# Kernel optimization log

Hardware: AMD Instinct MI355X
Metric: run time of the kernel (lower is better)

Reference implementation:

```python
import jax, jax.numpy as jnp
import numpy as np

DIM = 1024

def setup_inputs() -> dict:
    key = jax.random.key(0)
    k1, k2, k3, k4, k5 = jax.random.split(key, 5)
    x = jax.random.normal(k1, (8, 2048, DIM), dtype=jnp.float32)
    # nn.Linear-style params: W is [out, in], b is [out]
    s = 1.0 / np.sqrt(DIM)
    W1 = jax.random.uniform(k2, (DIM, DIM), jnp.float32, -s, s)
    b1 = jax.random.uniform(k3, (DIM,), jnp.float32, -s, s)
    W2 = jax.random.uniform(k4, (DIM, DIM), jnp.float32, -s, s)
    b2 = jax.random.uniform(k5, (DIM,), jnp.float32, -s, s)
    return {"x": x, "W1": W1, "b1": b1, "W2": W2, "b2": b2}

def reference(x, W1, b1, W2, b2):
    # NOTE: original module reuses linear_1 for BOTH V and Q (linear_3 unused)
    V = x @ W1.T + b1                      # [B,S,D]
    K = x @ W2.T + b2                      # [B,S,D]
    Q = x @ W1.T + b1                      # [B,S,D]
    scale = 1.0 / jnp.sqrt(jnp.float32(x.shape[-1]))
    scores = jnp.einsum('bkd,bqd->bkq', K, Q) * scale  # K @ Q^T, [B,S,S]
    attn = jax.nn.softmax(scores, axis=-1)
    out = jnp.einsum('bkq,bqd->bkd', attn, V)
    return out
```

## Files before the change

kernel.cpp:

```cpp
#include <hip/hip_runtime.h>
#include <hip/hip_fp16.h>
#include <cstdint>
#include <cstddef>

#define DIMK 1024
#define NBATCH 8
#define SEQ 2048

typedef _Float16 half8 __attribute__((ext_vector_type(8)));
typedef _Float16 half4_t __attribute__((ext_vector_type(4)));
typedef float float4_t __attribute__((ext_vector_type(4)));

__device__ __forceinline__ void gload16(const _Float16* g, _Float16* l) {
  __builtin_amdgcn_global_load_lds((const __attribute__((address_space(1))) void*)g,
                                   (__attribute__((address_space(3))) void*)l, 16, 0, 0);
}

#define BAR() asm volatile("s_barrier" ::: "memory")
#define LGKM(n) asm volatile("s_waitcnt lgkmcnt(" #n ")" ::: "memory")
#define VMW(n) asm volatile("s_waitcnt vmcnt(" #n ")" ::: "memory")
#define PRIO1() __builtin_amdgcn_s_setprio(1)
#define PRIO0() __builtin_amdgcn_s_setprio(0)
#define SCHED0() __builtin_amdgcn_sched_barrier(0)

__device__ __forceinline__ void gemm256_core(
    const char* __restrict__ Ab, const char* __restrict__ Bb,
    const int ldA, const int ldB, const int NT, _Float16* lds,
    float4_t (&acc)[8][4])
{
  const int tid = threadIdx.x;
  const int lane = tid & 63, wave = tid >> 6;
  const int warp_m = wave >> 2, warp_n = wave & 3;
  const int srow = lane >> 3;
  const int scb = ((lane & 7) ^ srow) << 4;
  const int c0 = wave * 2;
  const int fr = lane & 15, fg = lane >> 4, rsw = lane & 7;

  const int xo0 = (fg ^ rsw) << 3;
  const int xo1 = ((4 + fg) ^ rsw) << 3;
  const int aro = (warp_m * 64 + fr) * 64;
  const int bro = 16384 + (warp_n * 32 + fr) * 64;

  _Float16* const sA = lds + c0 * 512;
  _Float16* const sB = lds + 16384 + c0 * 512;
  const char* const gA = Ab + (size_t)(c0 * 8 + srow) * ldA + scb;
  const char* const gB = Bb + (size_t)(c0 * 8 + srow) * ldB + scb;
  const size_t ldA8 = (size_t)ldA * 8,   ldB8 = (size_t)ldB * 8;
  const size_t ldA128 = (size_t)ldA * 128, ldB128 = (size_t)ldB * 128;

  half8 AfLo[4][2], AfHi[4][2], Bf0[2][2], Bf1[2][2];

#define STG_A(pbuf, ob_, bot) do { \
    _Float16* _lb = sA + (pbuf) + ((bot) ? 8192 : 0); \
    const char* _g = gA + ((bot) ? ldA128 : 0) + (size_t)(ob_); \
    gload16((const _Float16*)_g, _lb); \
    gload16((const _Float16*)(_g + ldA8), _lb + 512); } while (0)
#define STG_B(pbuf, ob_, bot) do { \
    _Float16* _lb = sB + (pbuf) + ((bot) ? 8192 : 0); \
    const char* _g = gB + ((bot) ? ldB128 : 0) + (size_t)(ob_); \
    gload16((const _Float16*)_g, _lb); \
    gload16((const _Float16*)(_g + ldB8), _lb + 512); } while (0)

#define RDA(DST, pbase, g) do { \
    _Pragma("unroll") for (int m = 0; m < 4; ++m) { \
      DST[m][0] = *(const half8*)(lds + (pbase) + aro + (g) * 8192 + m * 1024 + xo0); \
      DST[m][1] = *(const half8*)(lds + (pbase) + aro + (g) * 8192 + m * 1024 + xo1); \
    } } while (0)
#define RDB(DST, pbase, g) do { \
    _Pragma("unroll") for (int n = 0; n < 2; ++n) { \
      DST[n][0] = *(const half8*)(lds + (pbase) + bro + (g) * 8192 + n * 1024 + xo0); \
      DST[n][1] = *(const half8*)(lds + (pbase) + bro + (g) * 8192 + n * 1024 + xo1); \
    } } while (0)

#define QUAD(gm, gn, AF, BF) do { \
    _Pragma("unroll") for (int m = 0; m < 4; ++m) \
    _Pragma("unroll") for (int n = 0; n < 2; ++n) \
    _Pragma("unroll") for (int kk = 0; kk < 2; ++kk) \
      acc[(gm) * 4 + m][(gn) * 2 + n] = __builtin_amdgcn_mfma_f32_16x16x32_f16( \
          AF[m][kk], BF[n][kk], acc[(gm) * 4 + m][(gn) * 2 + n], 0, 0, 0); \
  } while (0)

  STG_A(0, 0, 0); STG_B(0, 0, 0); STG_B(0, 0, 1); STG_A(0, 0, 1);
  STG_A(32768, 128, 0); STG_B(32768, 128, 0); STG_B(32768, 128, 1);
  VMW(8);
  BAR();
  RDA(AfLo, 0, 0);
  RDB(Bf0, 0, 0);

  int t = 0;
  for (; t + 2 < NT; ++t) {
    const int pb = (t & 1) << 15, pbn = pb ^ 32768;
    const int o1 = (t + 1) << 7, o2 = (t + 2) << 7;
    VMW(6);
    RDB(Bf1, pb, 1);
    LGKM(4); SCHED0();
    PRIO1(); QUAD(0, 0, AfLo, Bf0); PRIO0();
    STG_A(pbn, o1, 1);
    BAR();
    RDA(AfHi, pb, 1);
    LGKM(8); SCHED0();
    PRIO1(); QUAD(0, 1, AfLo, Bf1); PRIO0();
    STG_A(pb, o2, 0);
    BAR();
    VMW(6);
    LGKM(0); SCHED0();
    PRIO1(); QUAD(1, 1, AfHi, Bf1); PRIO0();
    STG_B(pb, o2, 0);
    BAR();
    PRIO1(); QUAD(1, 0, AfHi, Bf0); PRIO0();
    RDA(AfLo, pbn, 0);
    RDB(Bf0, pbn, 0);
    VMW(6);
    STG_B(pb, o2, 1);
    BAR();
  }
  {
    const int pb = (t & 1) << 15, pbn = pb ^ 32768;
    const int oL = (NT - 1) << 7;
    VMW(6);
    RDB(Bf1, pb, 1);
    LGKM(4); SCHED0();
    PRIO1(); QUAD(0, 0, AfLo, Bf0); PRIO0();
    STG_A(pbn, oL, 1);
    BAR();
    RDA(AfHi, pb, 1);
    LGKM(8); SCHED0();
    PRIO1(); QUAD(0, 1, AfLo, Bf1); PRIO0();
    BAR();
    LGKM(0); SCHED0();
    PRIO1(); QUAD(1, 1, AfHi, Bf1); PRIO0();
    PRIO1(); QUAD(1, 0, AfHi, Bf0); PRIO0();
    VMW(0);
    BAR();
  }
  {
    const int pb = ((NT - 1) & 1) << 15;
    RDA(AfLo, pb, 0); RDB(Bf0, pb, 0); RDB(Bf1, pb, 1);
    QUAD(0, 0, AfLo, Bf0); QUAD(0, 1, AfLo, Bf1);
    RDA(AfHi, pb, 1);
    QUAD(1, 1, AfHi, Bf1); QUAD(1, 0, AfHi, Bf0);
  }
#undef STG_A
#undef STG_B
#undef RDA
#undef RDB
#undef QUAD
}

#define ROW_LOCAL(mi) (warp_m * 64 + ((mi) & 3) * 16 + (((mi) >> 2) ? 128 : 0))
#define COL_LOCAL(nj) (warp_n * 32 + (((nj) & 1) ? 16 : 0) + (((nj) >> 1) ? 128 : 0))

__global__ __launch_bounds__(256) void prep_kernel(const float* __restrict__ x,
                                                   const float* __restrict__ W1,
                                                   const float* __restrict__ W2,
                                                   _Float16* __restrict__ xh,
                                                   _Float16* __restrict__ Wcat) {
  int i = blockIdx.x * 256 + threadIdx.x;
  if (i < 4194304) {
    float4_t v = ((const float4_t*)x)[i];
    half4_t h; h[0]=(_Float16)v[0]; h[1]=(_Float16)v[1]; h[2]=(_Float16)v[2]; h[3]=(_Float16)v[3];
    ((half4_t*)xh)[i] = h;
  } else if (i < 4456448) {
    int j = i - 4194304;
    float4_t v = ((const float4_t*)W1)[j];
    half4_t h; h[0]=(_Float16)v[0]; h[1]=(_Float16)v[1]; h[2]=(_Float16)v[2]; h[3]=(_Float16)v[3];
    ((half4_t*)Wcat)[j] = h;
  } else if (i < 4718592) {
    int j = i - 4456448;
    float4_t v = ((const float4_t*)W2)[j];
    half4_t h; h[0]=(_Float16)v[0]; h[1]=(_Float16)v[1]; h[2]=(_Float16)v[2]; h[3]=(_Float16)v[3];
    ((half4_t*)(Wcat + 1048576))[j] = h;
  }
}

__global__ __launch_bounds__(512, 2) void gemm_vk_kernel(
    const _Float16* __restrict__ xh, const _Float16* __restrict__ Wcat,
    const float* __restrict__ b1, const float* __restrict__ b2,
    _Float16* __restrict__ Vbuf, _Float16* __restrict__ Kbuf,
    _Float16* __restrict__ Vt) {
  __shared__ _Float16 lds[65536];
  const int tid = threadIdx.x, lane = tid & 63, wave = tid >> 6;
  const int warp_m = wave >> 2, warp_n = wave & 3;
  const int fr = lane & 15, rb = (lane >> 4) * 4;
  const int flat = blockIdx.x;
  const int wg = (flat & 7) * 64 + (flat >> 3);
  const int bm = wg >> 3, bn = wg & 7;
  const bool isV = bn < 4;
  const float* bias = isV ? b1 : b2;
  const int ncol0 = (bn & 3) * 256;
  float bv[4];
#pragma unroll
  for (int nj = 0; nj < 4; ++nj) bv[nj] = bias[ncol0 + COL_LOCAL(nj) + fr];

  float4_t acc[8][4] = {};
  gemm256_core((const char*)(xh + (size_t)bm * 256 * DIMK),
               (const char*)(Wcat + (size_t)bn * 256 * DIMK),
               DIMK * 2, DIMK * 2, DIMK / 64, lds, acc);

  _Float16* dst = isV ? Vbuf : Kbuf;
#pragma unroll
  for (int mi = 0; mi < 8; ++mi) {
    const int row = bm * 256 + ROW_LOCAL(mi) + rb;
#pragma unroll
    for (int nj = 0; nj < 4; ++nj) {
      const int col = ncol0 + COL_LOCAL(nj) + fr;
#pragma unroll
      for (int r = 0; r < 4; ++r)
        dst[(size_t)(row + r) * DIMK + col] = (_Float16)(acc[mi][nj][r] + bv[nj]);
    }
  }
  if (isV) {
    __syncthreads();
#pragma unroll
    for (int mi = 0; mi < 8; ++mi) {
      const int q0 = ROW_LOCAL(mi) + rb;
#pragma unroll
      for (int nj = 0; nj < 4; ++nj) {
        const int d = COL_LOCAL(nj) + fr;
        const float bb = bv[nj];
#pragma unroll
        for (int r = 0; r < 4; ++r) {
          const int q = q0 + r;
          lds[d * 256 + ((((q >> 3) ^ d) & 31) << 3) + (q & 7)] = (_Float16)(acc[mi][nj][r] + bb);
        }
      }
    }
    __syncthreads();
    const int b = bm >> 3, qb = (bm & 7) * 256;
    const size_t vtb = ((size_t)b * DIMK + ncol0) * SEQ + qb;
#pragma unroll
    for (int i = 0; i < 16; ++i) {
      const int idx = tid + i * 512;
      const int d = idx >> 5, G = idx & 31;
      half8 v = *(const half8*)(lds + d * 256 + (((G ^ d) & 31) << 3));
      *(half8*)(Vt + vtb + (size_t)d * SEQ + G * 8) = v;
    }
  }
}

__global__ __launch_bounds__(512, 2) void gemm_scores_kernel(
    const _Float16* __restrict__ Kb, const _Float16* __restrict__ Vb,
    _Float16* __restrict__ P, float* __restrict__ rsum_part) {
  __shared__ _Float16 lds[65536];
  const int tid = threadIdx.x, lane = tid & 63, wave = tid >> 6;
  const int warp_m = wave >> 2, warp_n = wave & 3;
  const int fr = lane & 15, rb = (lane >> 4) * 4;
  const int flat = blockIdx.x;
  const int wg = (flat & 7) * 64 + (flat >> 3);
  const int b = wg >> 6, loc = wg & 63, bm = loc >> 3, bn = loc & 7;

  float4_t acc[8][4] = {};
  gemm256_core((const char*)(Kb + (size_t)(b * SEQ + bm * 256) * DIMK),
               (const char*)(Vb + (size_t)(b * SEQ + bn * 256) * DIMK),
               DIMK * 2, DIMK * 2, DIMK / 64, lds, acc);

  __syncthreads();
  float* part = (float*)lds;
  _Float16* Pb = P + (size_t)b * SEQ * SEQ;
#pragma unroll
  for (int mi = 0; mi < 8; ++mi) {
    const int rl = ROW_LOCAL(mi) + rb;
#pragma unroll
    for (int r = 0; r < 4; ++r) {
      float s = 0.f;
#pragma unroll
      for (int nj = 0; nj < 4; ++nj) {
        const int col = bn * 256 + COL_LOCAL(nj) + fr;
        const _Float16 ph = (_Float16)__expf(acc[mi][nj][r] * 0.03125f);
        Pb[(size_t)(bm * 256 + rl + r) * SEQ + col] = ph;
        s += (float)ph;
      }
      s += __shfl_xor(s, 1, 64);
      s += __shfl_xor(s, 2, 64);
      s += __shfl_xor(s, 4, 64);
      s += __shfl_xor(s, 8, 64);
      if (fr == 0) part[warp_n * 256 + rl + r] = s;
    }
  }
  __syncthreads();
  if (tid < 256) {
    const float s = part[tid] + part[256 + tid] + part[512 + tid] + part[768 + tid];
    rsum_part[((size_t)b * 8 + bn) * SEQ + bm * 256 + tid] = s;
  }
}

__global__ __launch_bounds__(512, 2) void gemm_out_kernel(
    const _Float16* __restrict__ P, const _Float16* __restrict__ Vt,
    const float* __restrict__ rsum_part, float* __restrict__ out) {
  __shared__ _Float16 lds[65536];
  const int tid = threadIdx.x, lane = tid & 63, wave = tid >> 6;
  const int warp_m = wave >> 2, warp_n = wave & 3;
  const int fr = lane & 15, rb = (lane >> 4) * 4;
  const int flat = blockIdx.x;
  const int wg = (flat & 7) * 32 + (flat >> 3);
  const int b = wg >> 5, loc = wg & 31, bm = loc >> 2, bn = loc & 3;

  float4_t acc[8][4] = {};
  gemm256_core((const char*)(P + (size_t)(b * SEQ + bm * 256) * SEQ),
               (const char*)(Vt + (size_t)(b * DIMK + bn * 256) * SEQ),
               SEQ * 2, SEQ * 2, SEQ / 64, lds, acc);

  __syncthreads();
  float* invf = (float*)lds;
  if (tid < 256) {
    const float* rp = rsum_part + (size_t)b * 8 * SEQ + bm * 256 + tid;
    float s = 0.f;
#pragma unroll
    for (int j = 0; j < 8; ++j) s += rp[j * SEQ];
    invf[tid] = __builtin_amdgcn_rcpf(s);
  }
  __syncthreads();

  float* ob = out + ((size_t)b * SEQ + bm * 256) * DIMK + bn * 256;
#pragma unroll
  for (int mi = 0; mi < 8; ++mi) {
#pragma unroll
    for (int r = 0; r < 4; ++r) {
      const int row = ROW_LOCAL(mi) + rb + r;
      const float inv = invf[row];
#pragma unroll
      for (int nj = 0; nj < 4; ++nj) {
        const int col = COL_LOCAL(nj) + fr;
        ob[(size_t)row * DIMK + col] = acc[mi][nj][r] * inv;
      }
    }
  }
}

extern "C" void kernel_launch(void* const* d_in, const int* in_sizes, int n_in,
                              void* d_out, int out_size, void* d_ws, size_t ws_size,
                              hipStream_t stream) {
  const float* x  = (const float*)d_in[0];
  const float* W1 = (const float*)d_in[1];
  const float* b1 = (const float*)d_in[2];
  const float* W2 = (const float*)d_in[3];
  const float* b2 = (const float*)d_in[4];
  float* out = (float*)d_out;

  char* ws = (char*)d_ws;
  _Float16* xh   = (_Float16*)(ws);
  _Float16* Pbuf = (_Float16*)(ws);
  _Float16* Vt   = (_Float16*)(ws + 67108864);
  _Float16* Vbuf = (_Float16*)(ws + 100663296);
  _Float16* Kbuf = (_Float16*)(ws + 134217728);
  _Float16* Wcat = (_Float16*)(ws + 167772160);
  float* rsum_part = (float*)(ws + 167772160);

  prep_kernel<<<18432, 256, 0, stream>>>(x, W1, W2, xh, Wcat);
  gemm_vk_kernel<<<512, 512, 0, stream>>>(xh, Wcat, b1, b2, Vbuf, Kbuf, Vt);
  gemm_scores_kernel<<<512, 512, 0, stream>>>(Kbuf, Vbuf, Pbuf, rsum_part);
  gemm_out_kernel<<<256, 512, 0, stream>>>(Pbuf, Vt, rsum_part, out);
}
```

Measured before the change: 327.1 us.

## Unroll GEMM main loop by two with ping-pong B fragments and earlier LDS prefetch

Restructures the double-buffered GEMM main loop into a two-tile unrolled steady state that alternates the roles of the two B fragment register sets. LDS reads for the next tile's A and B fragments are issued earlier, interleaved with MFMA quads instead of after them, and the vmcnt waits are retuned. The epilogue is rewritten to match the new fragment rotation. The aim is to hide LDS read latency behind MFMA work, at the cost of more complex wait-count bookkeeping that could race if a count is wrong.

```diff
diff --git a/kernel.cpp b/kernel.cpp
--- a/kernel.cpp
+++ b/kernel.cpp
@@ -80,18 +80,50 @@
           AF[m][kk], BF[n][kk], acc[(gm) * 4 + m][(gn) * 2 + n], 0, 0, 0); \
   } while (0)
 
+#define TILE_STEADY(t_, BLO, BHI) do { \
+    const int pb = ((t_) & 1) << 15, pbn = pb ^ 32768; \
+    const int o1 = ((t_) + 1) << 7, o2 = ((t_) + 2) << 7; \
+     \
+    RDB(BHI, pb, 1); \
+    LGKM(4); SCHED0(); \
+    PRIO1(); QUAD(0, 0, AfLo, BLO); PRIO0(); \
+    STG_A(pbn, o1, 1); \
+    BAR(); \
+     \
+    RDA(AfHi, pb, 1); \
+    LGKM(8); SCHED0(); \
+    PRIO1(); QUAD(0, 1, AfLo, BHI); PRIO0(); \
+    STG_A(pb, o2, 0); \
+    VMW(6); \
+    BAR(); \
+     \
+    RDA(AfLo, pbn, 0); \
+    LGKM(8); SCHED0(); \
+    PRIO1(); QUAD(1, 1, AfHi, BHI); PRIO0(); \
+    STG_B(pb, o2, 0); \
+    BAR(); \
+     \
+    RDB(BHI, pbn, 0); \
+    PRIO1(); QUAD(1, 0, AfHi, BLO); PRIO0(); \
+    VMW(4); \
+    STG_B(pb, o2, 1); \
+    BAR(); \
+  } while (0)
+
   STG_A(0, 0, 0); STG_B(0, 0, 0); STG_B(0, 0, 1); STG_A(0, 0, 1);
   STG_A(32768, 128, 0); STG_B(32768, 128, 0); STG_B(32768, 128, 1);
-  VMW(8);
+  VMW(6);
   BAR();
   RDA(AfLo, 0, 0);
   RDB(Bf0, 0, 0);
 
-  int t = 0;
-  for (; t + 2 < NT; ++t) {
-    const int pb = (t & 1) << 15, pbn = pb ^ 32768;
-    const int o1 = (t + 1) << 7, o2 = (t + 2) << 7;
-    VMW(6);
+  for (int t = 0; t + 4 <= NT; t += 2) {
+    TILE_STEADY(t, Bf0, Bf1);
+    TILE_STEADY(t + 1, Bf1, Bf0);
+  }
+  {
+    const int pb = ((NT - 2) & 1) << 15, pbn = pb ^ 32768;
+    const int o1 = (NT - 1) << 7;
     RDB(Bf1, pb, 1);
     LGKM(4); SCHED0();
     PRIO1(); QUAD(0, 0, AfLo, Bf0); PRIO0();
@@ -100,51 +132,35 @@
     RDA(AfHi, pb, 1);
     LGKM(8); SCHED0();
     PRIO1(); QUAD(0, 1, AfLo, Bf1); PRIO0();
-    STG_A(pb, o2, 0);
+    VMW(4);
     BAR();
-    VMW(6);
-    LGKM(0); SCHED0();
+    RDA(AfLo, pbn, 0);
+    LGKM(8); SCHED0();
     PRIO1(); QUAD(1, 1, AfHi, Bf1); PRIO0();
-    STG_B(pb, o2, 0);
     BAR();
-    PRIO1(); QUAD(1, 0, AfHi, Bf0); PRIO0();
-    RDA(AfLo, pbn, 0);
-    RDB(Bf0, pbn, 0);
-    VMW(6);
-    STG_B(pb, o2, 1);
-    BAR();
-  }
-  {
-    const int pb = (t & 1) << 15, pbn = pb ^ 32768;
-    const int oL = (NT - 1) << 7;
-    VMW(6);
-    RDB(Bf1, pb, 1);
-    LGKM(4); SCHED0();
-    PRIO1(); QUAD(0, 0, AfLo, Bf0); PRIO0();
-    STG_A(pbn, oL, 1);
-    BAR();
-    RDA(AfHi, pb, 1);
-    LGKM(8); SCHED0();
-    PRIO1(); QUAD(0, 1, AfLo, Bf1); PRIO0();
-    BAR();
-    LGKM(0); SCHED0();
-    PRIO1(); QUAD(1, 1, AfHi, Bf1); PRIO0();
+    RDB(Bf1, pbn, 0);
     PRIO1(); QUAD(1, 0, AfHi, Bf0); PRIO0();
     VMW(0);
     BAR();
   }
   {
     const int pb = ((NT - 1) & 1) << 15;
-    RDA(AfLo, pb, 0); RDB(Bf0, pb, 0); RDB(Bf1, pb, 1);
-    QUAD(0, 0, AfLo, Bf0); QUAD(0, 1, AfLo, Bf1);
+    RDB(Bf0, pb, 1);
+    LGKM(4); SCHED0();
+    QUAD(0, 0, AfLo, Bf1);
     RDA(AfHi, pb, 1);
-    QUAD(1, 1, AfHi, Bf1); QUAD(1, 0, AfHi, Bf0);
+    LGKM(8); SCHED0();
+    QUAD(0, 1, AfLo, Bf0);
+    LGKM(0); SCHED0();
+    QUAD(1, 1, AfHi, Bf0);
+    QUAD(1, 0, AfHi, Bf1);
   }
 #undef STG_A
 #undef STG_B
 #undef RDA
 #undef RDB
 #undef QUAD
+#undef TILE_STEADY
 }
 
 #define ROW_LOCAL(mi) (warp_m * 64 + ((mi) & 3) * 16 + (((mi) >> 2) ? 128 : 0))
```

New measurement: 381.8 us. 1.17x slower.

## Reschedule GEMM mainloop to prefetch next-tile LDS fragments earlier with rotating B buffers

Applied to the files above, without the earlier changes.

Reorders the software-pipelined GEMM main loop so that LDS reads of the next tile's A and B fragments are issued one quadrant earlier, interleaved with the MFMA quadrants. B fragments rotate through a copy from Bf1 into Bf0 instead of a separate reload. Vmcnt waits are moved to just before each barrier, and the epilogue is restructured to match the new pipeline. This aims to hide LDS read latency and global-load waits behind MFMA work, at the cost of extra register moves, more live registers, and more delicate waitcnt correctness.

```diff
diff --git a/kernel.cpp b/kernel.cpp
--- a/kernel.cpp
+++ b/kernel.cpp
@@ -80,71 +80,89 @@
           AF[m][kk], BF[n][kk], acc[(gm) * 4 + m][(gn) * 2 + n], 0, 0, 0); \
   } while (0)
 
+#define BCOPY() do { \
+    _Pragma("unroll") for (int n = 0; n < 2; ++n) \
+    _Pragma("unroll") for (int k = 0; k < 2; ++k) Bf0[n][k] = Bf1[n][k]; \
+  } while (0)
+
   STG_A(0, 0, 0); STG_B(0, 0, 0); STG_B(0, 0, 1); STG_A(0, 0, 1);
   STG_A(32768, 128, 0); STG_B(32768, 128, 0); STG_B(32768, 128, 1);
-  VMW(8);
+  VMW(6);
   BAR();
   RDA(AfLo, 0, 0);
   RDB(Bf0, 0, 0);
 
-  int t = 0;
-  for (; t + 2 < NT; ++t) {
+  for (int t = 0; t + 2 < NT; ++t) {
     const int pb = (t & 1) << 15, pbn = pb ^ 32768;
     const int o1 = (t + 1) << 7, o2 = (t + 2) << 7;
-    VMW(6);
     RDB(Bf1, pb, 1);
-    LGKM(4); SCHED0();
+    SCHED0();
     PRIO1(); QUAD(0, 0, AfLo, Bf0); PRIO0();
     STG_A(pbn, o1, 1);
-    BAR();
+    VMW(8); BAR();
     RDA(AfHi, pb, 1);
+    STG_A(pb, o2, 0);
     LGKM(8); SCHED0();
     PRIO1(); QUAD(0, 1, AfLo, Bf1); PRIO0();
-    STG_A(pb, o2, 0);
-    BAR();
-    VMW(6);
-    LGKM(0); SCHED0();
+    VMW(8); BAR();
+    RDA(AfLo, pbn, 0);
+    STG_B(pb, o2, 0);
+    LGKM(8); SCHED0();
     PRIO1(); QUAD(1, 1, AfHi, Bf1); PRIO0();
-    STG_B(pb, o2, 0);
-    BAR();
+    VMW(8); BAR();
+    RDB(Bf1, pbn, 0);
+    SCHED0();
     PRIO1(); QUAD(1, 0, AfHi, Bf0); PRIO0();
-    RDA(AfLo, pbn, 0);
-    RDB(Bf0, pbn, 0);
-    VMW(6);
+    SCHED0();
+    BCOPY();
     STG_B(pb, o2, 1);
-    BAR();
+    VMW(8); BAR();
   }
   {
-    const int pb = (t & 1) << 15, pbn = pb ^ 32768;
+    const int pb = ((NT - 2) & 1) << 15, pbn = pb ^ 32768;
     const int oL = (NT - 1) << 7;
-    VMW(6);
     RDB(Bf1, pb, 1);
-    LGKM(4); SCHED0();
+    SCHED0();
     PRIO1(); QUAD(0, 0, AfLo, Bf0); PRIO0();
     STG_A(pbn, oL, 1);
-    BAR();
+    VMW(8); BAR();
+
     RDA(AfHi, pb, 1);
     LGKM(8); SCHED0();
     PRIO1(); QUAD(0, 1, AfLo, Bf1); PRIO0();
-    BAR();
-    LGKM(0); SCHED0();
+    VMW(6); BAR();
+
+    RDA(AfLo, pbn, 0);
+    LGKM(8); SCHED0();
     PRIO1(); QUAD(1, 1, AfHi, Bf1); PRIO0();
+    VMW(4); BAR();
+
+    RDB(Bf1, pbn, 0);
+    SCHED0();
     PRIO1(); QUAD(1, 0, AfHi, Bf0); PRIO0();
-    VMW(0);
-    BAR();
+    SCHED0();
+    BCOPY();
+    VMW(2); BAR();
   }
   {
     const int pb = ((NT - 1) & 1) << 15;
-    RDA(AfLo, pb, 0); RDB(Bf0, pb, 0); RDB(Bf1, pb, 1);
-    QUAD(0, 0, AfLo, Bf0); QUAD(0, 1, AfLo, Bf1);
+    RDB(Bf1, pb, 1);
+    SCHED0();
+    PRIO1(); QUAD(0, 0, AfLo, Bf0); PRIO0();
+    VMW(0); BAR();
+
     RDA(AfHi, pb, 1);
-    QUAD(1, 1, AfHi, Bf1); QUAD(1, 0, AfHi, Bf0);
+    LGKM(8); SCHED0();
+    PRIO1(); QUAD(0, 1, AfLo, Bf1); PRIO0();
+    LGKM(0); SCHED0();
+    PRIO1(); QUAD(1, 1, AfHi, Bf1); QUAD(1, 0, AfHi, Bf0); PRIO0();
   }
 #undef STG_A
 #undef STG_B
 #undef RDA
 #undef RDB
 #undef QUAD
+#undef BCOPY
 }
 
 #define ROW_LOCAL(mi) (warp_m * 64 + ((mi) & 3) * 16 + (((mi) >> 2) ? 128 : 0))
```

After: 329.0 us. No clear change (+0.6%).
